# Performance work log

Hardware: AMD Instinct MI355X
Metric: run time of the kernel (lower is better)

Reference implementation:

```python
import jax, jax.numpy as jnp
import numpy as np

B, L, D = 8, 256, 256
HN = 8            # head_num
HS = D // HN      # head_size
NEG = jnp.float32(-2.0**32 + 1)


def _split_heads(x):
    # torch.cat(torch.split(x, HS, dim=2), dim=0): head-major -> [HN*B, L, HS]
    b, l, _ = x.shape
    return x.reshape(b, l, HN, HS).transpose(2, 0, 1, 3).reshape(HN * b, l, HS)


def _split_heads_tm(t):
    # [B, L, L, D] -> [HN*B, L, L, HS], head-major on axis 0
    b, l, _, _ = t.shape
    return t.reshape(b, l, l, HN, HS).transpose(3, 0, 1, 2, 4).reshape(HN * b, l, l, HS)


def setup_inputs() -> dict:
    key = jax.random.key(0)
    ks = jax.random.split(key, 12)
    inp = {
        "queries": jax.random.normal(ks[0], (B, L, D), jnp.float32),
        "keys": jax.random.normal(ks[1], (B, L, D), jnp.float32),
        "time_mask": jnp.zeros((B, L, L), jnp.bool_),
        "attn_mask": jnp.triu(jnp.ones((L, L), jnp.bool_), k=1),  # causal: mask future
        "time_matrix_K": jax.random.normal(ks[2], (B, L, L, D), jnp.float32) * 0.05,
        "time_matrix_V": jax.random.normal(ks[3], (B, L, L, D), jnp.float32) * 0.05,
        "abs_pos_K": jax.random.normal(ks[4], (B, L, D), jnp.float32),
        "abs_pos_V": jax.random.normal(ks[5], (B, L, D), jnp.float32),
        "Q_w": jax.random.normal(ks[6], (D, D), jnp.float32) / np.sqrt(D),
        "Q_b": jnp.zeros((D,), jnp.float32),
        "K_w": jax.random.normal(ks[7], (D, D), jnp.float32) / np.sqrt(D),
        "K_b": jnp.zeros((D,), jnp.float32),
        "V_w": jax.random.normal(ks[8], (D, D), jnp.float32) / np.sqrt(D),
        "V_b": jnp.zeros((D,), jnp.float32),
    }
    return inp


def reference(queries, keys, time_mask, attn_mask, time_matrix_K, time_matrix_V,
              abs_pos_K, abs_pos_V, Q_w, Q_b, K_w, K_b, V_w, V_b):
    Q = queries @ Q_w.T + Q_b
    K = keys @ K_w.T + K_b
    V = keys @ V_w.T + V_b

    Q_, K_, V_ = _split_heads(Q), _split_heads(K), _split_heads(V)          # [HN*B, L, HS]
    tK_, tV_ = _split_heads_tm(time_matrix_K), _split_heads_tm(time_matrix_V)  # [HN*B, L, L, HS]
    pK_, pV_ = _split_heads(abs_pos_K), _split_heads(abs_pos_V)

    attn = jnp.einsum('bid,bjd->bij', Q_, K_)
    attn += jnp.einsum('bid,bjd->bij', Q_, pK_)
    attn += jnp.einsum('blij,blj->bli', tK_, Q_)
    attn = attn / jnp.sqrt(jnp.float32(HS))

    # NOTE: original expands time_mask batch-major (repeat_interleave) while
    # attn is head-major; reproduced faithfully.
    tm = jnp.repeat(time_mask, HN, axis=0)                # [B*HN, L, L]
    am = jnp.broadcast_to(attn_mask[None], attn.shape)
    attn = jnp.where(tm | am, NEG, attn)
    attn = jax.nn.softmax(attn, axis=-1)

    out = attn @ V_
    out += attn @ pV_
    out += jnp.einsum('bij,bijh->bih', attn, tV_)         # [HN*B, L, HS]

    # torch.cat(torch.split(out, B, dim=0), dim=2)
    out = out.reshape(HN, B, L, HS).transpose(1, 2, 0, 3).reshape(B, L, D)
    return out
```

## Files before the change

### kernel.cpp

```cpp
#include <hip/hip_runtime.h>
#include <math.h>

#define Bq 8
#define Lq 256
#define Dq 256
#define HNq 8
#define HSq 32
#define PADq 260

typedef float f4 __attribute__((ext_vector_type(4)));

#define PROJ_ROWS 8

__global__ __launch_bounds__(256) void proj_kernel(
    const float* __restrict__ queries, const float* __restrict__ keys,
    const float* __restrict__ apK, const float* __restrict__ apV,
    const float* __restrict__ Qw, const float* __restrict__ Qb,
    const float* __restrict__ Kw, const float* __restrict__ Kb,
    const float* __restrict__ Vw, const float* __restrict__ Vb,
    float* __restrict__ Q, float* __restrict__ KpK, float* __restrict__ VpV)
{
    __shared__ float inq[PROJ_ROWS][Dq];
    __shared__ float ink[PROJ_ROWS][Dq];
    const int r0 = blockIdx.x * PROJ_ROWS;
    const int tid = threadIdx.x;

    for (int idx = tid; idx < PROJ_ROWS * Dq; idx += 256) {
        int r = idx >> 8, c = idx & 255;
        inq[r][c] = queries[(size_t)(r0 + r) * Dq + c];
        ink[r][c] = keys[(size_t)(r0 + r) * Dq + c];
    }
    __syncthreads();

    const int d = tid;
    float aq[PROJ_ROWS], ak[PROJ_ROWS], av[PROJ_ROWS];
#pragma unroll
    for (int r = 0; r < PROJ_ROWS; ++r) { aq[r] = 0.f; ak[r] = 0.f; av[r] = 0.f; }

    const float4* qwr = (const float4*)(Qw + (size_t)d * Dq);
    const float4* kwr = (const float4*)(Kw + (size_t)d * Dq);
    const float4* vwr = (const float4*)(Vw + (size_t)d * Dq);

    for (int k4 = 0; k4 < Dq / 4; ++k4) {
        float4 wq = qwr[k4], wk = kwr[k4], wv = vwr[k4];
        int k = k4 * 4;
#pragma unroll
        for (int r = 0; r < PROJ_ROWS; ++r) {
            float i0 = inq[r][k], i1 = inq[r][k + 1], i2 = inq[r][k + 2], i3 = inq[r][k + 3];
            aq[r] += i0 * wq.x + i1 * wq.y + i2 * wq.z + i3 * wq.w;
            float j0 = ink[r][k], j1 = ink[r][k + 1], j2 = ink[r][k + 2], j3 = ink[r][k + 3];
            ak[r] += j0 * wk.x + j1 * wk.y + j2 * wk.z + j3 * wk.w;
            av[r] += j0 * wv.x + j1 * wv.y + j2 * wv.z + j3 * wv.w;
        }
    }

    const float qb = Qb[d], kb = Kb[d], vb = Vb[d];
#pragma unroll
    for (int r = 0; r < PROJ_ROWS; ++r) {
        size_t o = (size_t)(r0 + r) * Dq + d;
        Q[o]   = (aq[r] + qb) * 0.17677669529663687f;
        KpK[o] = ak[r] + kb + apK[o];
        VpV[o] = av[r] + vb + apV[o];
    }
}

__global__ __launch_bounds__(256) void attn_kernel(
    const float* __restrict__ Q, const float* __restrict__ KpK,
    const float* __restrict__ VpV,
    const float* __restrict__ tmK, const float* __restrict__ tmV,
    float* __restrict__ out)
{
    const int id  = blockIdx.x;
    const int b   = id & 7;
    const int x   = id >> 3;
    const int i1  = x;
    const int i2  = Lq - 1 - x;

    const int tid  = threadIdx.x;
    const int w    = tid >> 6;
    const int lane = tid & 63;
    const int h    = lane >> 3;
    const int l8   = lane & 7;
    const int c4   = lane * 4;

    __shared__ float qs[2][Dq];
    __shared__ float sb[2][HNq * PADq];
    __shared__ float po[2][4][Dq];

    const size_t rowB = (size_t)b * Lq * Dq;

    if (tid < 128) {
        int r = tid >> 6, qi = tid & 63;
        ((f4*)qs[r])[qi] =
            *((const f4*)(Q + rowB + (size_t)(r ? i2 : i1) * Dq) + qi);
    }
    __syncthreads();
    const f4 qa = *(const f4*)(qs[0] + c4);
    const f4 qb4 = *(const f4*)(qs[1] + c4);

    const float* tk1 = tmK + ((size_t)(b * Lq + i1) * Lq) * Dq;
    const float* tk2 = tmK + ((size_t)(b * Lq + i2) * Lq) * Dq;
    const float* tv1 = tmV + ((size_t)(b * Lq + i1) * Lq) * Dq;
    const float* tv2 = tmV + ((size_t)(b * Lq + i2) * Lq) * Dq;

    for (int j = w; j <= i2; j += 4) {
        f4 kp = *(const f4*)(KpK + rowB + (size_t)j * Dq + c4);
        f4 t2 = __builtin_nontemporal_load((const f4*)(tk2 + (size_t)j * Dq + c4));
        float s2 = qb4[0] * (t2[0] + kp[0]) + qb4[1] * (t2[1] + kp[1])
                 + qb4[2] * (t2[2] + kp[2]) + qb4[3] * (t2[3] + kp[3]);
        s2 += __shfl_xor(s2, 1);
        s2 += __shfl_xor(s2, 2);
        s2 += __shfl_xor(s2, 4);
        if (l8 == 0) sb[1][h * PADq + j] = s2;
        if (j <= i1) {
            f4 t1 = __builtin_nontemporal_load((const f4*)(tk1 + (size_t)j * Dq + c4));
            float s1 = qa[0] * (t1[0] + kp[0]) + qa[1] * (t1[1] + kp[1])
                     + qa[2] * (t1[2] + kp[2]) + qa[3] * (t1[3] + kp[3]);
            s1 += __shfl_xor(s1, 1);
            s1 += __shfl_xor(s1, 2);
            s1 += __shfl_xor(s1, 4);
            if (l8 == 0) sb[0][h * PADq + j] = s1;
        }
    }
    __syncthreads();

    {
        const int r  = tid >> 7;
        const int hh = (tid >> 4) & 7;
        const int jl = tid & 15;
        const int i  = r ? i2 : i1;
        float* sr = &sb[r][hh * PADq];
        float vv[16];
        float m = -3.0e38f;
#pragma unroll
        for (int k = 0; k < 16; ++k) {
            int j = jl + 16 * k;
            vv[k] = (j <= i) ? sr[j] : -3.0e38f;
            m = fmaxf(m, vv[k]);
        }
#pragma unroll
        for (int off = 8; off >= 1; off >>= 1) m = fmaxf(m, __shfl_xor(m, off));
        float sum = 0.f;
#pragma unroll
        for (int k = 0; k < 16; ++k) { vv[k] = __expf(vv[k] - m); sum += vv[k]; }
#pragma unroll
        for (int off = 8; off >= 1; off >>= 1) sum += __shfl_xor(sum, off);
        const float inv = 1.0f / sum;
#pragma unroll
        for (int k = 0; k < 16; ++k) sr[jl + 16 * k] = vv[k] * inv;
    }
    __syncthreads();

    f4 a1 = {0.f, 0.f, 0.f, 0.f};
    f4 a2 = {0.f, 0.f, 0.f, 0.f};
    for (int j = w; j <= i2; j += 4) {
        f4 vp = *(const f4*)(VpV + rowB + (size_t)j * Dq + c4);
        f4 t2 = __builtin_nontemporal_load((const f4*)(tv2 + (size_t)j * Dq + c4));
        a2 += sb[1][h * PADq + j] * (t2 + vp);
        if (j <= i1) {
            f4 t1 = __builtin_nontemporal_load((const f4*)(tv1 + (size_t)j * Dq + c4));
            a1 += sb[0][h * PADq + j] * (t1 + vp);
        }
    }
    *(f4*)(po[0][w] + c4) = a1;
    *(f4*)(po[1][w] + c4) = a2;
    __syncthreads();

    out[rowB + (size_t)i1 * Dq + tid] =
        po[0][0][tid] + po[0][1][tid] + po[0][2][tid] + po[0][3][tid];
    out[rowB + (size_t)i2 * Dq + tid] =
        po[1][0][tid] + po[1][1][tid] + po[1][2][tid] + po[1][3][tid];
}

extern "C" void kernel_launch(void* const* d_in, const int* in_sizes, int n_in,
                              void* d_out, int out_size, void* d_ws, size_t ws_size,
                              hipStream_t stream) {
    const float* queries = (const float*)d_in[0];
    const float* keys    = (const float*)d_in[1];
    const float* tmK = (const float*)d_in[4];
    const float* tmV = (const float*)d_in[5];
    const float* apK = (const float*)d_in[6];
    const float* apV = (const float*)d_in[7];
    const float* Qw  = (const float*)d_in[8];
    const float* Qb  = (const float*)d_in[9];
    const float* Kw  = (const float*)d_in[10];
    const float* Kb  = (const float*)d_in[11];
    const float* Vw  = (const float*)d_in[12];
    const float* Vb  = (const float*)d_in[13];
    float* out = (float*)d_out;

    const size_t n = (size_t)Bq * Lq * Dq;
    float* Q   = (float*)d_ws;
    float* KpK = Q + n;
    float* VpV = KpK + n;

    proj_kernel<<<dim3((Bq * Lq) / PROJ_ROWS), 256, 0, stream>>>(
        queries, keys, apK, apV, Qw, Qb, Kw, Kb, Vw, Vb, Q, KpK, VpV);

    attn_kernel<<<dim3(Bq * Lq / 2), 256, 0, stream>>>(
        Q, KpK, VpV, tmK, tmV, out);
}
```

Before: 165.7 us.

## Split attention over two key halves with a log-sum-exp combine kernel

```diff
diff --git a/kernel.cpp b/kernel.cpp
--- a/kernel.cpp
+++ b/kernel.cpp
@@ -6,7 +6,7 @@
 #define Dq 256
 #define HNq 8
 #define HSq 32
-#define PADq 260
+#define PADs 132
 
 typedef float f4 __attribute__((ext_vector_type(4)));
 
@@ -64,17 +64,18 @@
     }
 }
 
-__global__ __launch_bounds__(256) void attn_kernel(
+__global__ __launch_bounds__(256) void attn_part(
     const float* __restrict__ Q, const float* __restrict__ KpK,
     const float* __restrict__ VpV,
     const float* __restrict__ tmK, const float* __restrict__ tmV,
-    float* __restrict__ out)
+    float* __restrict__ pacc, float* __restrict__ pm, float* __restrict__ pl)
 {
-    const int id  = blockIdx.x;
-    const int b   = id & 7;
-    const int x   = id >> 3;
-    const int i1  = x;
-    const int i2  = Lq - 1 - x;
+    const int id = blockIdx.x;
+    const int b  = id & 7;
+    const int s  = (id >> 3) & 1;
+    const int x  = id >> 4;
+    const int i1 = x;
+    const int i2 = Lq - 1 - x;
 
     const int tid  = threadIdx.x;
     const int w    = tid >> 6;
@@ -84,7 +85,7 @@
     const int c4   = lane * 4;
 
     __shared__ float qs[2][Dq];
-    __shared__ float sb[2][HNq * PADq];
+    __shared__ float sb[2][HNq * PADs];
     __shared__ float po[2][4][Dq];
 
     const size_t rowB = (size_t)b * Lq * Dq;
@@ -95,7 +96,7 @@
             *((const f4*)(Q + rowB + (size_t)(r ? i2 : i1) * Dq) + qi);
     }
     __syncthreads();
-    const f4 qa = *(const f4*)(qs[0] + c4);
+    const f4 qa  = *(const f4*)(qs[0] + c4);
     const f4 qb4 = *(const f4*)(qs[1] + c4);
 
     const float* tk1 = tmK + ((size_t)(b * Lq + i1) * Lq) * Dq;
@@ -103,7 +104,8 @@
     const float* tv1 = tmV + ((size_t)(b * Lq + i1) * Lq) * Dq;
     const float* tv2 = tmV + ((size_t)(b * Lq + i2) * Lq) * Dq;
 
-    for (int j = w; j <= i2; j += 4) {
+#pragma unroll 2
+    for (int j = 4 * s + w, lj = w; j <= i2; j += 8, lj += 4) {
         f4 kp = *(const f4*)(KpK + rowB + (size_t)j * Dq + c4);
         f4 t2 = __builtin_nontemporal_load((const f4*)(tk2 + (size_t)j * Dq + c4));
         float s2 = qb4[0] * (t2[0] + kp[0]) + qb4[1] * (t2[1] + kp[1])
@@ -111,7 +113,7 @@
         s2 += __shfl_xor(s2, 1);
         s2 += __shfl_xor(s2, 2);
         s2 += __shfl_xor(s2, 4);
-        if (l8 == 0) sb[1][h * PADq + j] = s2;
+        if (l8 == 0) sb[1][h * PADs + lj] = s2;
         if (j <= i1) {
             f4 t1 = __builtin_nontemporal_load((const f4*)(tk1 + (size_t)j * Dq + c4));
             float s1 = qa[0] * (t1[0] + kp[0]) + qa[1] * (t1[1] + kp[1])
@@ -119,7 +121,7 @@
             s1 += __shfl_xor(s1, 1);
             s1 += __shfl_xor(s1, 2);
             s1 += __shfl_xor(s1, 4);
-            if (l8 == 0) sb[0][h * PADq + j] = s1;
+            if (l8 == 0) sb[0][h * PADs + lj] = s1;
         }
     }
     __syncthreads();
@@ -129,47 +131,81 @@
         const int hh = (tid >> 4) & 7;
         const int jl = tid & 15;
         const int i  = r ? i2 : i1;
-        float* sr = &sb[r][hh * PADq];
-        float vv[16];
+        float* sr = &sb[r][hh * PADs];
+        float vv[8];
         float m = -3.0e38f;
 #pragma unroll
-        for (int k = 0; k < 16; ++k) {
-            int j = jl + 16 * k;
-            vv[k] = (j <= i) ? sr[j] : -3.0e38f;
-            m = fmaxf(m, vv[k]);
+        for (int t = 0; t < 8; ++t) {
+            int lj = jl + 16 * t;
+            int j  = ((lj >> 2) << 3) + 4 * s + (lj & 3);
+            vv[t] = (j <= i) ? sr[lj] : -3.0e38f;
+            m = fmaxf(m, vv[t]);
         }
 #pragma unroll
         for (int off = 8; off >= 1; off >>= 1) m = fmaxf(m, __shfl_xor(m, off));
-        float sum = 0.f;
-#pragma unroll
-        for (int k = 0; k < 16; ++k) { vv[k] = __expf(vv[k] - m); sum += vv[k]; }
-#pragma unroll
-        for (int off = 8; off >= 1; off >>= 1) sum += __shfl_xor(sum, off);
-        const float inv = 1.0f / sum;
-#pragma unroll
-        for (int k = 0; k < 16; ++k) sr[jl + 16 * k] = vv[k] * inv;
+        float l = 0.f;
+#pragma unroll
+        for (int t = 0; t < 8; ++t) {
+            int lj = jl + 16 * t;
+            int j  = ((lj >> 2) << 3) + 4 * s + (lj & 3);
+            float p = (j <= i) ? __expf(vv[t] - m) : 0.f;
+            sr[lj] = p;
+            l += p;
+        }
+#pragma unroll
+        for (int off = 8; off >= 1; off >>= 1) l += __shfl_xor(l, off);
+        if (jl == 0) {
+            size_t o = ((size_t)s * (Bq * Lq) + (size_t)b * Lq + i) * HNq + hh;
+            pm[o] = m;
+            pl[o] = l;
+        }
     }
     __syncthreads();
 
     f4 a1 = {0.f, 0.f, 0.f, 0.f};
     f4 a2 = {0.f, 0.f, 0.f, 0.f};
-    for (int j = w; j <= i2; j += 4) {
+#pragma unroll 2
+    for (int j = 4 * s + w, lj = w; j <= i2; j += 8, lj += 4) {
         f4 vp = *(const f4*)(VpV + rowB + (size_t)j * Dq + c4);
         f4 t2 = __builtin_nontemporal_load((const f4*)(tv2 + (size_t)j * Dq + c4));
-        a2 += sb[1][h * PADq + j] * (t2 + vp);
+        a2 += sb[1][h * PADs + lj] * (t2 + vp);
         if (j <= i1) {
             f4 t1 = __builtin_nontemporal_load((const f4*)(tv1 + (size_t)j * Dq + c4));
-            a1 += sb[0][h * PADq + j] * (t1 + vp);
+            a1 += sb[0][h * PADs + lj] * (t1 + vp);
         }
     }
     *(f4*)(po[0][w] + c4) = a1;
     *(f4*)(po[1][w] + c4) = a2;
     __syncthreads();
 
-    out[rowB + (size_t)i1 * Dq + tid] =
-        po[0][0][tid] + po[0][1][tid] + po[0][2][tid] + po[0][3][tid];
-    out[rowB + (size_t)i2 * Dq + tid] =
-        po[1][0][tid] + po[1][1][tid] + po[1][2][tid] + po[1][3][tid];
+    {
+        float o0 = po[0][0][tid] + po[0][1][tid] + po[0][2][tid] + po[0][3][tid];
+        float o1 = po[1][0][tid] + po[1][1][tid] + po[1][2][tid] + po[1][3][tid];
+        size_t r0o = (size_t)s * (Bq * Lq) + (size_t)b * Lq + i1;
+        size_t r1o = (size_t)s * (Bq * Lq) + (size_t)b * Lq + i2;
+        pacc[r0o * Dq + tid] = o0;
+        pacc[r1o * Dq + tid] = o1;
+    }
+}
+
+__global__ __launch_bounds__(256) void attn_combine(
+    const float* __restrict__ pacc, const float* __restrict__ pm,
+    const float* __restrict__ pl, float* __restrict__ out)
+{
+    const int rb = blockIdx.x;
+    const int d  = threadIdx.x;
+    const int h  = d >> 5;
+
+    const size_t o0 = (size_t)rb * HNq + h;
+    const size_t o1 = (size_t)(Bq * Lq + rb) * HNq + h;
+    float m0 = pm[o0], m1 = pm[o1];
+    float l0 = pl[o0], l1 = pl[o1];
+    float M  = fmaxf(m0, m1);
+    float e0 = __expf(m0 - M), e1 = __expf(m1 - M);
+    float L  = l0 * e0 + l1 * e1;
+    float num = pacc[(size_t)rb * Dq + d] * e0
+              + pacc[(size_t)(Bq * Lq + rb) * Dq + d] * e1;
+    out[(size_t)rb * Dq + d] = num / L;
 }
 
 extern "C" void kernel_launch(void* const* d_in, const int* in_sizes, int n_in,
@@ -190,13 +226,18 @@
     float* out = (float*)d_out;
 
     const size_t n = (size_t)Bq * Lq * Dq;
-    float* Q   = (float*)d_ws;
-    float* KpK = Q + n;
-    float* VpV = KpK + n;
+    float* Q    = (float*)d_ws;
+    float* KpK  = Q + n;
+    float* VpV  = KpK + n;
+    float* pacc = VpV + n;
+    float* pm   = pacc + (size_t)2 * Bq * Lq * Dq;
+    float* pl   = pm + (size_t)2 * Bq * Lq * HNq;
 
     proj_kernel<<<dim3((Bq * Lq) / PROJ_ROWS), 256, 0, stream>>>(
         queries, keys, apK, apV, Qw, Qb, Kw, Kb, Vw, Vb, Q, KpK, VpV);
 
-    attn_kernel<<<dim3(Bq * Lq / 2), 256, 0, stream>>>(
-        Q, KpK, VpV, tmK, tmV, out);
-}
+    attn_part<<<dim3(Bq * Lq), 256, 0, stream>>>(
+        Q, KpK, VpV, tmK, tmV, pacc, pm, pl);
+
+    attn_combine<<<dim3(Bq * Lq), 256, 0, stream>>>(pacc, pm, pl, out);
+}
```

Measured after the change: 160.4 us (median of 2 runs). -3.2%, faster.

## Split dense QK and PV terms into separate tiled GEMM kernels

Applied to the files above, without the earlier changes.

```diff
diff --git a/kernel.cpp b/kernel.cpp
--- a/kernel.cpp
+++ b/kernel.cpp
@@ -9,6 +9,7 @@
 #define PADq 260
 
 typedef float f4 __attribute__((ext_vector_type(4)));
+#define NTL(p) __builtin_nontemporal_load((const f4*)(p))
 
 #define PROJ_ROWS 8
 
@@ -64,9 +65,48 @@
     }
 }
 
+__global__ __launch_bounds__(256) void gemm_s2(
+    const float* __restrict__ Q, const float* __restrict__ KpK,
+    float* __restrict__ SP)
+{
+    const int blk = blockIdx.x;
+    const int bh  = blk >> 2;
+    const int b   = bh >> 3, h = bh & 7;
+    const int i0  = (blk & 3) * 64;
+    const int tid = threadIdx.x;
+
+    __shared__ float Kl[256][33];
+    __shared__ float Ql[64][36];
+
+    for (int idx = tid; idx < 256 * 32; idx += 256) {
+        int j = idx >> 5, d = idx & 31;
+        Kl[j][d] = KpK[((size_t)(b * Lq + j)) * Dq + h * HSq + d];
+    }
+    for (int idx = tid; idx < 64 * 32; idx += 256) {
+        int il = idx >> 5, d = idx & 31;
+        Ql[il][d] = Q[((size_t)(b * Lq + i0 + il)) * Dq + h * HSq + d];
+    }
+    __syncthreads();
+
+    float kr[32];
+#pragma unroll
+    for (int d = 0; d < 32; ++d) kr[d] = Kl[tid][d];
+
+    float* srow = SP + ((size_t)(b * HNq + h) * Lq + i0) * Lq + tid;
+    for (int il = 0; il < 64; ++il) {
+        float s = 0.f;
+#pragma unroll
+        for (int d8 = 0; d8 < 8; ++d8) {
+            f4 q = *(const f4*)&Ql[il][d8 * 4];
+            s += q[0] * kr[d8*4] + q[1] * kr[d8*4+1]
+               + q[2] * kr[d8*4+2] + q[3] * kr[d8*4+3];
+        }
+        srow[(size_t)il * Lq] = s;
+    }
+}
+
 __global__ __launch_bounds__(256) void attn_kernel(
-    const float* __restrict__ Q, const float* __restrict__ KpK,
-    const float* __restrict__ VpV,
+    const float* __restrict__ Q, float* __restrict__ SP,
     const float* __restrict__ tmK, const float* __restrict__ tmV,
     float* __restrict__ out)
 {
@@ -95,7 +135,7 @@
             *((const f4*)(Q + rowB + (size_t)(r ? i2 : i1) * Dq) + qi);
     }
     __syncthreads();
-    const f4 qa = *(const f4*)(qs[0] + c4);
+    const f4 qa  = *(const f4*)(qs[0] + c4);
     const f4 qb4 = *(const f4*)(qs[1] + c4);
 
     const float* tk1 = tmK + ((size_t)(b * Lq + i1) * Lq) * Dq;
@@ -104,18 +144,15 @@
     const float* tv2 = tmV + ((size_t)(b * Lq + i2) * Lq) * Dq;
 
     for (int j = w; j <= i2; j += 4) {
-        f4 kp = *(const f4*)(KpK + rowB + (size_t)j * Dq + c4);
-        f4 t2 = __builtin_nontemporal_load((const f4*)(tk2 + (size_t)j * Dq + c4));
-        float s2 = qb4[0] * (t2[0] + kp[0]) + qb4[1] * (t2[1] + kp[1])
-                 + qb4[2] * (t2[2] + kp[2]) + qb4[3] * (t2[3] + kp[3]);
+        f4 t2 = NTL(tk2 + (size_t)j * Dq + c4);
+        float s2 = qb4[0]*t2[0] + qb4[1]*t2[1] + qb4[2]*t2[2] + qb4[3]*t2[3];
         s2 += __shfl_xor(s2, 1);
         s2 += __shfl_xor(s2, 2);
         s2 += __shfl_xor(s2, 4);
         if (l8 == 0) sb[1][h * PADq + j] = s2;
         if (j <= i1) {
-            f4 t1 = __builtin_nontemporal_load((const f4*)(tk1 + (size_t)j * Dq + c4));
-            float s1 = qa[0] * (t1[0] + kp[0]) + qa[1] * (t1[1] + kp[1])
-                     + qa[2] * (t1[2] + kp[2]) + qa[3] * (t1[3] + kp[3]);
+            f4 t1 = NTL(tk1 + (size_t)j * Dq + c4);
+            float s1 = qa[0]*t1[0] + qa[1]*t1[1] + qa[2]*t1[2] + qa[3]*t1[3];
             s1 += __shfl_xor(s1, 1);
             s1 += __shfl_xor(s1, 2);
             s1 += __shfl_xor(s1, 4);
@@ -130,12 +167,13 @@
         const int jl = tid & 15;
         const int i  = r ? i2 : i1;
         float* sr = &sb[r][hh * PADq];
+        float* spRow = SP + ((size_t)(b * HNq + hh) * Lq + i) * Lq;
         float vv[16];
         float m = -3.0e38f;
 #pragma unroll
         for (int k = 0; k < 16; ++k) {
             int j = jl + 16 * k;
-            vv[k] = (j <= i) ? sr[j] : -3.0e38f;
+            vv[k] = (j <= i) ? (sr[j] + spRow[j]) : -3.0e38f;
             m = fmaxf(m, vv[k]);
         }
 #pragma unroll
@@ -147,19 +185,23 @@
         for (int off = 8; off >= 1; off >>= 1) sum += __shfl_xor(sum, off);
         const float inv = 1.0f / sum;
 #pragma unroll
-        for (int k = 0; k < 16; ++k) sr[jl + 16 * k] = vv[k] * inv;
+        for (int k = 0; k < 16; ++k) {
+            int j = jl + 16 * k;
+            float p = vv[k] * inv;
+            sr[j] = p;
+            spRow[j] = p;
+        }
     }
     __syncthreads();
 
     f4 a1 = {0.f, 0.f, 0.f, 0.f};
     f4 a2 = {0.f, 0.f, 0.f, 0.f};
     for (int j = w; j <= i2; j += 4) {
-        f4 vp = *(const f4*)(VpV + rowB + (size_t)j * Dq + c4);
-        f4 t2 = __builtin_nontemporal_load((const f4*)(tv2 + (size_t)j * Dq + c4));
-        a2 += sb[1][h * PADq + j] * (t2 + vp);
+        f4 t2 = NTL(tv2 + (size_t)j * Dq + c4);
+        a2 += sb[1][h * PADq + j] * t2;
         if (j <= i1) {
-            f4 t1 = __builtin_nontemporal_load((const f4*)(tv1 + (size_t)j * Dq + c4));
-            a1 += sb[0][h * PADq + j] * (t1 + vp);
+            f4 t1 = NTL(tv1 + (size_t)j * Dq + c4);
+            a1 += sb[0][h * PADq + j] * t1;
         }
     }
     *(f4*)(po[0][w] + c4) = a1;
@@ -170,6 +212,56 @@
         po[0][0][tid] + po[0][1][tid] + po[0][2][tid] + po[0][3][tid];
     out[rowB + (size_t)i2 * Dq + tid] =
         po[1][0][tid] + po[1][1][tid] + po[1][2][tid] + po[1][3][tid];
+}
+
+__global__ __launch_bounds__(256) void gemm_pv(
+    const float* __restrict__ SP, const float* __restrict__ VpV,
+    float* __restrict__ out)
+{
+    const int blk = blockIdx.x;
+    const int bh  = blk >> 2;
+    const int b   = bh >> 3, h = bh & 7;
+    const int i0  = (blk & 3) * 64;
+    const int tid = threadIdx.x;
+
+    __shared__ float Vl[256][32];
+    __shared__ float Pl[64][65];
+
+    for (int idx = tid; idx < 256 * 32; idx += 256) {
+        int j = idx >> 5, d = idx & 31;
+        Vl[j][d] = VpV[((size_t)(b * Lq + j)) * Dq + h * HSq + d];
+    }
+
+    const int il = tid >> 2;
+    const int d0 = (tid & 3) * 8;
+    float acc[8];
+#pragma unroll
+    for (int dd = 0; dd < 8; ++dd) acc[dd] = 0.f;
+
+    const float* prow = SP + ((size_t)(b * HNq + h) * Lq + i0) * Lq;
+
+    for (int jt = 0; jt < 4; ++jt) {
+        __syncthreads();
+        for (int idx = tid; idx < 64 * 64; idx += 256) {
+            int pil = idx >> 6, jj = idx & 63;
+            Pl[pil][jj] = prow[(size_t)pil * Lq + jt * 64 + jj];
+        }
+        __syncthreads();
+        for (int jj = 0; jj < 64; ++jj) {
+            float p = Pl[il][jj];
+            int j = jt * 64 + jj;
+            f4 v0 = *(const f4*)&Vl[j][d0];
+            f4 v1 = *(const f4*)&Vl[j][d0 + 4];
+            acc[0] += p * v0[0]; acc[1] += p * v0[1];
+            acc[2] += p * v0[2]; acc[3] += p * v0[3];
+            acc[4] += p * v1[0]; acc[5] += p * v1[1];
+            acc[6] += p * v1[2]; acc[7] += p * v1[3];
+        }
+    }
+
+    size_t o = ((size_t)(b * Lq + i0 + il)) * Dq + h * HSq + d0;
+#pragma unroll
+    for (int dd = 0; dd < 8; ++dd) out[o + dd] += acc[dd];
 }
 
 extern "C" void kernel_launch(void* const* d_in, const int* in_sizes, int n_in,
@@ -193,10 +285,15 @@
     float* Q   = (float*)d_ws;
     float* KpK = Q + n;
     float* VpV = KpK + n;
+    float* SP  = VpV + n;
 
     proj_kernel<<<dim3((Bq * Lq) / PROJ_ROWS), 256, 0, stream>>>(
         queries, keys, apK, apV, Qw, Qb, Kw, Kb, Vw, Vb, Q, KpK, VpV);
 
+    gemm_s2<<<dim3(256), 256, 0, stream>>>(Q, KpK, SP);
+
     attn_kernel<<<dim3(Bq * Lq / 2), 256, 0, stream>>>(
-        Q, KpK, VpV, tmK, tmV, out);
-}
+        Q, SP, tmK, tmV, out);
+
+    gemm_pv<<<dim3(256), 256, 0, stream>>>(SP, VpV, out);
+}
```

Measured after the change: 217.1 us. 1.31x slower.
